# Optimization experiments

Measured on AMD Instinct MI355X. Metric: run time of the kernel, lower is better.

Reference implementation:

```python
import jax, jax.numpy as jnp
import numpy as np

N_NODES = 131072
B_GRAPHS = 16
L_MAX = 8192  # nodes per graph (equal partition -> static dense shape)
CHANNELS = 512
HEAD_CH = 128  # head_channels, heads fixed to 1


def _to_dense_batch(x, batch, num_graphs, max_nodes):
    # Mirrors torch_geometric.utils.to_dense_batch for a sorted batch vector.
    n = x.shape[0]
    counts = jnp.zeros((num_graphs,), jnp.int32).at[batch].add(1)
    offsets = jnp.concatenate([jnp.zeros((1,), jnp.int32), jnp.cumsum(counts)[:-1]])
    pos = jnp.arange(n, dtype=jnp.int32) - offsets[batch]
    dense = jnp.zeros((num_graphs, max_nodes, x.shape[1]), x.dtype).at[batch, pos].set(x)
    mask = jnp.zeros((num_graphs, max_nodes), bool).at[batch, pos].set(True)
    return dense, mask


def setup_inputs() -> dict:
    key = jax.random.key(0)
    kx, kq, kk, kv = jax.random.split(key, 4)
    x = jax.random.normal(kx, (N_NODES, CHANNELS), jnp.float32)
    scale = 1.0 / np.sqrt(CHANNELS)
    Wq = jax.random.normal(kq, (HEAD_CH, CHANNELS), jnp.float32) * scale
    Wk = jax.random.normal(kk, (HEAD_CH, CHANNELS), jnp.float32) * scale
    Wv = jax.random.normal(kv, (HEAD_CH, CHANNELS), jnp.float32) * scale
    # sorted batch vector: equal-size graphs so L_MAX is static
    batch = (jnp.arange(N_NODES, dtype=jnp.int32) // L_MAX).astype(jnp.int32)
    return {"x": x, "Wq": Wq, "Wk": Wk, "Wv": Wv, "batch": batch,
            "num_graphs": B_GRAPHS, "max_nodes": L_MAX}


def reference(x, Wq, Wk, Wv, batch, num_graphs, max_nodes):
    B, L, H, M = num_graphs, max_nodes, 1, Wq.shape[0]
    xd, mask = _to_dense_batch(x, batch, B, L)  # [B, L, C]; padded rows are zero
    qs = (xd @ Wq.T).reshape(B, L, H, M)
    ks = (xd @ Wk.T).reshape(B, L, H, M)
    vs = (xd @ Wv.T).reshape(B, L, H, M)
    # GLOBAL (scalar) Frobenius norm, as in torch.norm(t, p=2)
    qs = qs / jnp.linalg.norm(qs)
    ks = ks / jnp.linalg.norm(ks)
    n_const = qs.shape[0]  # source uses qs.shape[0] (= batch size) here
    # linear attention: K^T V first, then Q (K^T V)
    kvs = jnp.einsum('blhm,blhd->bhmd', ks, vs)
    attention_num = jnp.einsum('bnhm,bhmd->bnhd', qs, kvs) + n_const * vs
    ks_sum = ks.sum(axis=1)  # [B, H, M]
    attention_normalizer = jnp.einsum('bnhm,bhm->bnh', qs, ks_sum)[..., None] + n_const
    attn_output = attention_num / attention_normalizer  # [B, L, H, M]
    return attn_output
```

## Files before the change

### kernel.cpp

```cpp
#include <hip/hip_runtime.h>
#include <hip/hip_bf16.h>

typedef __bf16 bf16;
typedef __bf16 bf16x4 __attribute__((ext_vector_type(4)));
typedef __bf16 bf16x8 __attribute__((ext_vector_type(8)));
typedef float f32x4 __attribute__((ext_vector_type(4)));

#define N_NODES 131072
#define CH      512
#define HD      128
#define LMAX    8192
#define NG      16

typedef __attribute__((address_space(3))) unsigned int lds_u32;
typedef __attribute__((address_space(1))) const unsigned int g_u32;

__device__ __forceinline__ void gload16(const void* gp, void* lp) {
    __builtin_amdgcn_global_load_lds((g_u32*)gp, (lds_u32*)lp, 16, 0, 0);
}

__global__ __launch_bounds__(256, 1) void k0_prep(
    const float* __restrict__ Wq, const float* __restrict__ Wk,
    const float* __restrict__ Wv, bf16* __restrict__ wsW)
{
    int t = blockIdx.x * 256 + threadIdx.x;
    int c = t / 3072;
    int r = t % 3072;
    int j = r >> 3, g = r & 7;
    const float* Wrow = (j < 128) ? (Wq + (size_t)j * CH)
                       : (j < 256) ? (Wk + (size_t)(j - 128) * CH)
                                   : (Wv + (size_t)(j - 256) * CH);
    int col0 = (g ^ (j & 7)) << 3;
    const float* src = Wrow + c * 64 + col0;
    float4 f0 = *(const float4*)src;
    float4 f1 = *(const float4*)(src + 4);
    bf16x8 o;
    o[0] = (bf16)f0.x; o[1] = (bf16)f0.y; o[2] = (bf16)f0.z; o[3] = (bf16)f0.w;
    o[4] = (bf16)f1.x; o[5] = (bf16)f1.y; o[6] = (bf16)f1.z; o[7] = (bf16)f1.w;
    *(bf16x8*)(wsW + (size_t)t * 8) = o;
}

__global__ __launch_bounds__(256, 1) void k1_proj(
    const float* __restrict__ x, const bf16* __restrict__ wsW,
    bf16* __restrict__ qo, bf16* __restrict__ ko, bf16* __restrict__ vo,
    float* __restrict__ sumsq)
{
    __shared__ float A32[2][2048];
    __shared__ bf16 Bs[24576];
    __shared__ float rq[4], rk[4];

    const int tid = threadIdx.x;
    const int lane = tid & 63;
    const int w = tid >> 6;
    const int lr = lane & 15, lh = lane >> 4;
    const int n0 = blockIdx.x * 64;

    const int as_row = lane >> 3;
    const int as_col = (((lane & 7) ^ as_row) << 2);
    const size_t abase = (size_t)(n0 + as_row) * CH + as_col;

    f32x4 acc[4][6];
    #pragma unroll
    for (int mi = 0; mi < 4; mi++)
        #pragma unroll
        for (int ni = 0; ni < 6; ni++)
            acc[mi][ni] = (f32x4){0.f, 0.f, 0.f, 0.f};

    {
        const char* wb = (const char*)wsW + w * 1024 + lane * 16;
        char* db = (char*)Bs + w * 1024;
        #pragma unroll
        for (int i = 0; i < 12; i++) gload16(wb + i * 4096, db + i * 4096);
        #pragma unroll
        for (int i = 0; i < 2; i++) {
            int jc = w * 2 + i;
            gload16((const char*)(x + abase + (size_t)jc * 8 * CH),
                    (char*)&A32[0][jc * 256]);
        }
        __syncthreads();
    }

    for (int a = 0; a < 16; a++) {
        const int cur = a & 1, nxt = cur ^ 1;
        const int kk = (a & 1) * 32;
        if (a < 15) {
            #pragma unroll
            for (int i = 0; i < 2; i++) {
                int jc = w * 2 + i;
                gload16((const char*)(x + abase + (size_t)jc * 8 * CH + (a + 1) * 32),
                        (char*)&A32[nxt][jc * 256]);
            }
        }
        bf16x8 af[4];
        #pragma unroll
        for (int mi = 0; mi < 4; mi++) {
            int r = mi * 16 + lr;
            int base = r * 32;
            f32x4 lo = *(const f32x4*)&A32[cur][base + ((( lh * 2     ) ^ (lr & 7)) << 2)];
            f32x4 hi = *(const f32x4*)&A32[cur][base + (((lh * 2 + 1) ^ (lr & 7)) << 2)];
            bf16x8 t;
            t[0] = (bf16)lo[0]; t[1] = (bf16)lo[1]; t[2] = (bf16)lo[2]; t[3] = (bf16)lo[3];
            t[4] = (bf16)hi[0]; t[5] = (bf16)hi[1]; t[6] = (bf16)hi[2]; t[7] = (bf16)hi[3];
            af[mi] = t;
        }
        #pragma unroll
        for (int ni = 0; ni < 6; ni++) {
            int j = w * 96 + ni * 16 + lr;
            bf16x8 bf_ = *(const bf16x8*)&Bs[j * 64 + ((kk + lh * 8) ^ ((j & 7) << 3))];
            #pragma unroll
            for (int mi = 0; mi < 4; mi++)
                acc[mi][ni] = __builtin_amdgcn_mfma_f32_16x16x32_bf16(
                    af[mi], bf_, acc[mi][ni], 0, 0, 0);
        }
        __syncthreads();
        if ((a & 1) && a < 15) {
            const char* wb = (const char*)wsW + (size_t)((a >> 1) + 1) * 49152
                           + w * 1024 + lane * 16;
            char* db = (char*)Bs + w * 1024;
            #pragma unroll
            for (int i = 0; i < 12; i++) gload16(wb + i * 4096, db + i * 4096);
            __syncthreads();
        }
    }

    float sq = 0.f, sk = 0.f;
    #pragma unroll
    for (int mi = 0; mi < 4; mi++) {
        #pragma unroll
        for (int ni = 0; ni < 6; ni++) {
            int col = w * 96 + ni * 16 + lr;
            int arr = col >> 7, cc = col & 127;
            bf16* dst = (arr == 0) ? qo : (arr == 1) ? ko : vo;
            #pragma unroll
            for (int r = 0; r < 4; r++) {
                int row = n0 + mi * 16 + lh * 4 + r;
                float val = acc[mi][ni][r];
                dst[(size_t)row * HD + cc] = (bf16)val;
                if (arr == 0) sq += val * val;
                else if (arr == 1) sk += val * val;
            }
        }
    }
    #pragma unroll
    for (int off = 32; off > 0; off >>= 1) {
        sq += __shfl_down(sq, off);
        sk += __shfl_down(sk, off);
    }
    if (lane == 0) { rq[w] = sq; rk[w] = sk; }
    __syncthreads();
    if (tid == 0) {
        float a = 0.f, b = 0.f;
        #pragma unroll
        for (int i = 0; i < 4; i++) { a += rq[i]; b += rk[i]; }
        atomicAdd(&sumsq[0], a);
        atomicAdd(&sumsq[1], b);
    }
}

__global__ __launch_bounds__(512, 1) void k2_kv(
    const bf16* __restrict__ ko, const bf16* __restrict__ vo,
    float* __restrict__ part_kv, float* __restrict__ part_ks)
{
    __shared__ __align__(16) char smem[16640];
    bf16 (*kt)[130] = (bf16(*)[130])smem;
    bf16 (*vt)[130] = (bf16(*)[130])(smem + 8320);
    float* scr = (float*)smem;

    const int tid = threadIdx.x, lane = tid & 63, w = tid >> 6;
    const int wr = w >> 2, wc = w & 3;
    const int lr = lane & 15, lh = lane >> 4;
    const int b = blockIdx.x >> 4, cch = blockIdx.x & 15;
    const size_t l0 = (size_t)b * LMAX + (size_t)cch * 512;
    const int sr = tid >> 4, sc = tid & 15;

    f32x4 acc[4][2];
    #pragma unroll
    for (int mi = 0; mi < 4; mi++)
        #pragma unroll
        for (int ni = 0; ni < 2; ni++)
            acc[mi][ni] = (f32x4){0.f, 0.f, 0.f, 0.f};
    float ks8[8] = {};

    uint4 kk4 = *(const uint4*)&ko[(l0 + sr) * HD + sc * 8];
    uint4 vv4 = *(const uint4*)&vo[(l0 + sr) * HD + sc * 8];

    for (int lt = 0; lt < 512; lt += 32) {
        __syncthreads();
        #pragma unroll
        for (int j2 = 0; j2 < 4; j2++) {
            *(unsigned int*)&kt[sr][sc * 8 + j2 * 2] = ((const unsigned int*)&kk4)[j2];
            *(unsigned int*)&vt[sr][sc * 8 + j2 * 2] = ((const unsigned int*)&vv4)[j2];
        }
        #pragma unroll
        for (int j = 0; j < 8; j++) ks8[j] += (float)((const bf16*)&kk4)[j];
        __syncthreads();
        if (lt + 32 < 512) {
            kk4 = *(const uint4*)&ko[(l0 + lt + 32 + sr) * HD + sc * 8];
            vv4 = *(const uint4*)&vo[(l0 + lt + 32 + sr) * HD + sc * 8];
        }
        bf16x8 a[4], bb[2];
        #pragma unroll
        for (int mi = 0; mi < 4; mi++) {
            int m = wr * 64 + mi * 16 + lr;
            #pragma unroll
            for (int j = 0; j < 8; j++) a[mi][j] = kt[lh * 8 + j][m];
        }
        #pragma unroll
        for (int ni = 0; ni < 2; ni++) {
            int d = wc * 32 + ni * 16 + lr;
            #pragma unroll
            for (int j = 0; j < 8; j++) bb[ni][j] = vt[lh * 8 + j][d];
        }
        #pragma unroll
        for (int mi = 0; mi < 4; mi++)
            #pragma unroll
            for (int ni = 0; ni < 2; ni++)
                acc[mi][ni] = __builtin_amdgcn_mfma_f32_16x16x32_bf16(
                    a[mi], bb[ni], acc[mi][ni], 0, 0, 0);
    }

    __syncthreads();
    #pragma unroll
    for (int j = 0; j < 8; j++) scr[tid * 8 + j] = ks8[j];
    __syncthreads();
    if (tid < 128) {
        float s = 0.f;
        #pragma unroll
        for (int g = 0; g < 32; g++)
            s += scr[((g << 4) | (tid >> 3)) * 8 + (tid & 7)];
        part_ks[blockIdx.x * HD + tid] = s;
    }

    float* dst = part_kv + (size_t)blockIdx.x * 16384;
    #pragma unroll
    for (int mi = 0; mi < 4; mi++)
        #pragma unroll
        for (int ni = 0; ni < 2; ni++)
            #pragma unroll
            for (int r = 0; r < 4; r++) {
                int m = wr * 64 + mi * 16 + lh * 4 + r;
                int d = wc * 32 + ni * 16 + lr;
                dst[m * HD + d] = acc[mi][ni][r];
            }
}

__global__ __launch_bounds__(256, 1) void k2b_reduce(
    const float* __restrict__ part_kv, const float* __restrict__ part_ks,
    const float* __restrict__ sumsq,
    bf16* __restrict__ kvsT, float* __restrict__ ks_sum_s)
{
    const int b = blockIdx.x >> 3, ms = blockIdx.x & 7, tid = threadIdx.x;
    const float s_qk = rsqrtf(sumsq[0]) * rsqrtf(sumsq[1]);

    #pragma unroll
    for (int i = 0; i < 8; i++) {
        int idx = i * 256 + tid;
        int m = ms * 16 + (idx >> 7), d = idx & 127;
        float s = 0.f;
        #pragma unroll
        for (int c = 0; c < 16; c++)
            s += part_kv[((size_t)(b * 16 + c) << 14) + (m << 7) + d];
        kvsT[((size_t)b << 14) + (d << 7) + m] = (bf16)(s * s_qk);
    }
    if (ms == 0 && tid < 128) {
        float s = 0.f;
        #pragma unroll
        for (int c = 0; c < 16; c++)
            s += part_ks[(b * 16 + c) * HD + tid];
        ks_sum_s[b * HD + tid] = s * s_qk;
    }
}

__global__ __launch_bounds__(256, 2) void k3_out(
    const bf16* __restrict__ qo, const bf16* __restrict__ vo,
    const bf16* __restrict__ kvsT, const float* __restrict__ ks_sum_s,
    float* __restrict__ out)
{
    __shared__ bf16 qs[128][136];
    __shared__ bf16 vsh[128][136];
    __shared__ float kss[128];
    __shared__ float denom[128];
    const int tid = threadIdx.x, lane = tid & 63, w = tid >> 6;
    const int lr = lane & 15, lh = lane >> 4;
    const int n0 = blockIdx.x * 128;
    const int b = n0 >> 13;

    #pragma unroll
    for (int i = 0; i < 8; i++) {
        int idx = tid + i * 256;
        int r = idx >> 4, c8 = idx & 15;
        *(bf16x8*)&qs[r][c8 * 8]  = *(const bf16x8*)&qo[(size_t)(n0 + r) * HD + c8 * 8];
        *(bf16x8*)&vsh[r][c8 * 8] = *(const bf16x8*)&vo[(size_t)(n0 + r) * HD + c8 * 8];
    }
    if (tid < 128) kss[tid] = ks_sum_s[b * HD + tid];
    __syncthreads();

    if (tid < 128) {
        float s = 0.f;
        #pragma unroll 8
        for (int m = 0; m < HD; m++) s += (float)qs[tid][m] * kss[m];
        denom[tid] = s + 16.0f;
    }

    f32x4 acc[2][8];
    #pragma unroll
    for (int mi = 0; mi < 2; mi++)
        #pragma unroll
        for (int ni = 0; ni < 8; ni++)
            acc[mi][ni] = (f32x4){0.f, 0.f, 0.f, 0.f};

    #pragma unroll
    for (int k0 = 0; k0 < HD; k0 += 32) {
        bf16x8 a[2], bb[8];
        #pragma unroll
        for (int mi = 0; mi < 2; mi++)
            a[mi] = *(const bf16x8*)&qs[w * 32 + mi * 16 + lr][k0 + lh * 8];
        #pragma unroll
        for (int ni = 0; ni < 8; ni++)
            bb[ni] = *(const bf16x8*)&kvsT[(size_t)b * 16384 + (size_t)(ni * 16 + lr) * HD + k0 + lh * 8];
        #pragma unroll
        for (int mi = 0; mi < 2; mi++)
            #pragma unroll
            for (int ni = 0; ni < 8; ni++)
                acc[mi][ni] = __builtin_amdgcn_mfma_f32_16x16x32_bf16(
                    a[mi], bb[ni], acc[mi][ni], 0, 0, 0);
    }
    __syncthreads();

    #pragma unroll
    for (int mi = 0; mi < 2; mi++) {
        #pragma unroll
        for (int ni = 0; ni < 8; ni++) {
            int col = ni * 16 + lr;
            #pragma unroll
            for (int r = 0; r < 4; r++) {
                int row = w * 32 + mi * 16 + lh * 4 + r;
                float vv = (float)vsh[row][col];
                out[(size_t)(n0 + row) * HD + col] =
                    (acc[mi][ni][r] + 16.0f * vv) / denom[row];
            }
        }
    }
}

extern "C" void kernel_launch(void* const* d_in, const int* in_sizes, int n_in,
                              void* d_out, int out_size, void* d_ws, size_t ws_size,
                              hipStream_t stream)
{
    const float* x  = (const float*)d_in[0];
    const float* Wq = (const float*)d_in[1];
    const float* Wk = (const float*)d_in[2];
    const float* Wv = (const float*)d_in[3];

    char* ws = (char*)d_ws;
    const size_t Q_OFF   = 0;
    const size_t K_OFF   = 33554432;
    const size_t V_OFF   = 67108864;
    const size_t PKV_OFF = 100663296;
    const size_t PKS_OFF = 117440512;
    const size_t KVS_OFF = 117571584;
    const size_t KSS_OFF = 118095872;
    const size_t SSQ_OFF = 118104064;
    const size_t NEED    = 118104072;
    if (ws_size < NEED) return;

    bf16*  qo      = (bf16*)(ws + Q_OFF);
    bf16*  ko      = (bf16*)(ws + K_OFF);
    bf16*  vo      = (bf16*)(ws + V_OFF);
    float* part_kv = (float*)(ws + PKV_OFF);
    float* part_ks = (float*)(ws + PKS_OFF);
    bf16*  kvsT    = (bf16*)(ws + KVS_OFF);
    float* ks_sum  = (float*)(ws + KSS_OFF);
    float* sumsq   = (float*)(ws + SSQ_OFF);
    bf16*  wsW     = (bf16*)(ws + PKV_OFF);

    hipMemsetAsync(sumsq, 0, 8, stream);
    k0_prep<<<dim3(96), dim3(256), 0, stream>>>(Wq, Wk, Wv, wsW);
    k1_proj<<<dim3(N_NODES / 64), dim3(256), 0, stream>>>(x, wsW, qo, ko, vo, sumsq);
    k2_kv<<<dim3(256), dim3(512), 0, stream>>>(ko, vo, part_kv, part_ks);
    k2b_reduce<<<dim3(128), dim3(256), 0, stream>>>(part_kv, part_ks, sumsq, kvsT, ks_sum);
    k3_out<<<dim3(N_NODES / 128), dim3(256), 0, stream>>>(qo, vo, kvsT, ks_sum, (float*)d_out);
}
```

Measured before the change: 209.9 us.

## Double-buffer weight tiles per K-step and overlap prefetch with partial vmcnt waits

Projection weights are now staged in two smaller LDS buffers, one 32-wide K chunk each, instead of one 64-wide buffer that was reloaded every other iteration. The prep kernel's swizzle is rewritten to match the new chunk size. Each iteration issues the next A and B tile loads together, then waits with an explicit vmcnt(8) so the loads for the current step are complete while the new prefetch stays in flight. This removes the exposed weight reload and its extra barrier. The cost is more fragile hand-written waitcnt and barrier ordering, which the compiler can no longer reason about.

```diff
diff --git a/kernel.cpp b/kernel.cpp
--- a/kernel.cpp
+++ b/kernel.cpp
@@ -24,16 +24,15 @@
     const float* __restrict__ Wv, bf16* __restrict__ wsW)
 {
     int t = blockIdx.x * 256 + threadIdx.x;
-    int c = t / 3072;
-    int r = t % 3072;
-    int j = r >> 3, g = r & 7;
+    int c = t / 1536;
+    int r = t % 1536;
+    int j = r >> 2, g = r & 3;
     const float* Wrow = (j < 128) ? (Wq + (size_t)j * CH)
                        : (j < 256) ? (Wk + (size_t)(j - 128) * CH)
                                    : (Wv + (size_t)(j - 256) * CH);
-    int col0 = (g ^ (j & 7)) << 3;
-    const float* src = Wrow + c * 64 + col0;
-    float4 f0 = *(const float4*)src;
-    float4 f1 = *(const float4*)(src + 4);
+    int col0 = c * 32 + ((g ^ ((j >> 1) & 3)) << 3);
+    float4 f0 = *(const float4*)(Wrow + col0);
+    float4 f1 = *(const float4*)(Wrow + col0 + 4);
     bf16x8 o;
     o[0] = (bf16)f0.x; o[1] = (bf16)f0.y; o[2] = (bf16)f0.z; o[3] = (bf16)f0.w;
     o[4] = (bf16)f1.x; o[5] = (bf16)f1.y; o[6] = (bf16)f1.z; o[7] = (bf16)f1.w;
@@ -46,7 +45,7 @@
     float* __restrict__ sumsq)
 {
     __shared__ float A32[2][2048];
-    __shared__ bf16 Bs[24576];
+    __shared__ bf16 Bs[2][12288];
     __shared__ float rq[4], rk[4];
 
     const int tid = threadIdx.x;
@@ -68,35 +67,44 @@
 
     {
         const char* wb = (const char*)wsW + w * 1024 + lane * 16;
-        char* db = (char*)Bs + w * 1024;
-        #pragma unroll
-        for (int i = 0; i < 12; i++) gload16(wb + i * 4096, db + i * 4096);
+        char* db = (char*)&Bs[0][0] + w * 1024;
+        #pragma unroll
+        for (int i = 0; i < 6; i++) gload16(wb + i * 4096, db + i * 4096);
         #pragma unroll
         for (int i = 0; i < 2; i++) {
             int jc = w * 2 + i;
             gload16((const char*)(x + abase + (size_t)jc * 8 * CH),
                     (char*)&A32[0][jc * 256]);
         }
-        __syncthreads();
+        asm volatile("s_waitcnt vmcnt(0)\n\ts_barrier" ::: "memory");
+        __builtin_amdgcn_sched_barrier(0);
     }
 
     for (int a = 0; a < 16; a++) {
         const int cur = a & 1, nxt = cur ^ 1;
-        const int kk = (a & 1) * 32;
         if (a < 15) {
+            const char* wb = (const char*)wsW + (size_t)(a + 1) * 24576 + w * 1024 + lane * 16;
+            char* db = (char*)&Bs[nxt][0] + w * 1024;
+            #pragma unroll
+            for (int i = 0; i < 6; i++) gload16(wb + i * 4096, db + i * 4096);
             #pragma unroll
             for (int i = 0; i < 2; i++) {
                 int jc = w * 2 + i;
                 gload16((const char*)(x + abase + (size_t)jc * 8 * CH + (a + 1) * 32),
                         (char*)&A32[nxt][jc * 256]);
             }
-        }
+            asm volatile("s_waitcnt vmcnt(8)\n\ts_barrier" ::: "memory");
+        } else {
+            asm volatile("s_waitcnt vmcnt(0)\n\ts_barrier" ::: "memory");
+        }
+        __builtin_amdgcn_sched_barrier(0);
+
         bf16x8 af[4];
         #pragma unroll
         for (int mi = 0; mi < 4; mi++) {
             int r = mi * 16 + lr;
             int base = r * 32;
-            f32x4 lo = *(const f32x4*)&A32[cur][base + ((( lh * 2     ) ^ (lr & 7)) << 2)];
+            f32x4 lo = *(const f32x4*)&A32[cur][base + (((lh * 2    ) ^ (lr & 7)) << 2)];
             f32x4 hi = *(const f32x4*)&A32[cur][base + (((lh * 2 + 1) ^ (lr & 7)) << 2)];
             bf16x8 t;
             t[0] = (bf16)lo[0]; t[1] = (bf16)lo[1]; t[2] = (bf16)lo[2]; t[3] = (bf16)lo[3];
@@ -106,21 +114,15 @@
         #pragma unroll
         for (int ni = 0; ni < 6; ni++) {
             int j = w * 96 + ni * 16 + lr;
-            bf16x8 bf_ = *(const bf16x8*)&Bs[j * 64 + ((kk + lh * 8) ^ ((j & 7) << 3))];
+            int g = lh ^ ((j >> 1) & 3);
+            bf16x8 bf_ = *(const bf16x8*)&Bs[cur][j * 32 + (g << 3)];
             #pragma unroll
             for (int mi = 0; mi < 4; mi++)
                 acc[mi][ni] = __builtin_amdgcn_mfma_f32_16x16x32_bf16(
                     af[mi], bf_, acc[mi][ni], 0, 0, 0);
         }
-        __syncthreads();
-        if ((a & 1) && a < 15) {
-            const char* wb = (const char*)wsW + (size_t)((a >> 1) + 1) * 49152
-                           + w * 1024 + lane * 16;
-            char* db = (char*)Bs + w * 1024;
-            #pragma unroll
-            for (int i = 0; i < 12; i++) gload16(wb + i * 4096, db + i * 4096);
-            __syncthreads();
-        }
+        asm volatile("s_barrier" ::: "memory");
+        __builtin_amdgcn_sched_barrier(0);
     }
 
     float sq = 0.f, sk = 0.f;
```

Result: faster. 202.2 us (-3.6%).
